# Kernel optimization log

Measured on AMD Instinct MI355X. Metric: run time of the kernel, lower is better.

The kernel has to match this reference:

```python
import jax, jax.numpy as jnp
import numpy as np

N, E = 50000, 800000
IN_DIM, HID, OUT_DIM = 512, 64, 40


def setup_inputs() -> dict:
    key = jax.random.key(0)
    ks = jax.random.split(key, 7)
    X = jax.random.normal(ks[0], (N, IN_DIM), dtype=jnp.float32)
    edges = jax.random.randint(ks[1], (2, E), 0, N, dtype=jnp.int64)
    # GCNConv weight (glorot) and bias
    W1 = jax.random.normal(ks[2], (IN_DIM, HID), dtype=jnp.float32) / np.sqrt(IN_DIM)
    b1 = jnp.zeros((HID,), dtype=jnp.float32)
    # fc Linear
    Wfc = jax.random.normal(ks[3], (OUT_DIM, HID), dtype=jnp.float32) / np.sqrt(HID)
    bfc = jax.random.normal(ks[4], (OUT_DIM,), dtype=jnp.float32) * 0.01
    return {"X": X, "edges": edges, "W1": W1, "b1": b1, "Wfc": Wfc, "bfc": bfc}


def gcn_conv(x, src, dst, W, b, n):
    # PyG GCNConv: transform, add self-loops, symmetric D^-1/2 A D^-1/2 norm,
    # scatter-add messages at destination, add bias.
    h = x @ W  # [N, HID]
    loop = jnp.arange(n, dtype=src.dtype)
    src = jnp.concatenate([src, loop])
    dst = jnp.concatenate([dst, loop])
    deg = jax.ops.segment_sum(jnp.ones_like(dst, dtype=h.dtype), dst, num_segments=n)
    dinv = jnp.where(deg > 0, jax.lax.rsqrt(deg), 0.0)
    coef = dinv[src] * dinv[dst]  # [E+N]
    msgs = coef[:, None] * h[src]  # gather + scale
    agg = jax.ops.segment_sum(msgs, dst, num_segments=n)  # scatter-add
    return agg + b


def reference(X, edges, W1, b1, Wfc, bfc):
    n = X.shape[0]
    src, dst = edges[0], edges[1]
    h = jax.nn.relu(gcn_conv(X, src, dst, W1, b1, n))  # [N, HID]
    return h @ Wfc.T + bfc  # [N, OUT_DIM]
```

## Files before the change

### kernel.cpp

```cpp
#include <hip/hip_runtime.h>
#include <hip/hip_bf16.h>

typedef unsigned short u16;
typedef __bf16 bf16_8 __attribute__((ext_vector_type(8)));
typedef float f32_4 __attribute__((ext_vector_type(4)));

#define IN_DIM 512
#define HID 64
#define OUT_DIM 40
#define CAP 64
#define CF_BLOCKS 512

__global__ void k_prep(const float* __restrict__ W1, u16* __restrict__ W1t,
                       int* __restrict__ cnt, int n) {
    int i = blockIdx.x * 256 + threadIdx.x;
    if (i < n) cnt[i] = 0;
    if (i < IN_DIM * HID) {
        int k = i / HID, o = i % HID;
        __hip_bfloat16 v = __float2bfloat16(W1[i]);
        W1t[o * IN_DIM + k] = *reinterpret_cast<u16*>(&v);
    }
}

__launch_bounds__(256)
__global__ void k_work(const float* __restrict__ X, const u16* __restrict__ W1t,
                       const int* __restrict__ src, const int* __restrict__ dst,
                       int* cnt, u16* __restrict__ csr, u16* __restrict__ hs,
                       int N, int E, int NT) {
    __shared__ __align__(16) u16 As[2][64 * 72];
    const int t = threadIdx.x;

    if ((int)blockIdx.x >= NT) {
        int tid = ((int)blockIdx.x - NT) * 256 + t;
        int stride = CF_BLOCKS * 256;
        for (int e = tid; e < E; e += stride) {
            int d = dst[e];
            int p = atomicAdd(&cnt[d], 1);
            if (p < CAP) csr[(size_t)d * CAP + p] = (u16)src[e];
        }
        return;
    }

    const int wave = t >> 6;
    const int lane = t & 63;
    const int m = lane & 15;
    const int quad = lane >> 4;
    const int n0 = blockIdx.x * 64;

    f32_4 acc[4];
    #pragma unroll
    for (int c = 0; c < 4; c++) acc[c] = (f32_4){0.f, 0.f, 0.f, 0.f};

    const int r_st = t >> 2;
    const int c2 = t & 3;

    int row = n0 + r_st; if (row >= N) row = N - 1;
    const float* xp = X + (size_t)row * IN_DIM + c2 * 16;

    f32_4 x0 = *reinterpret_cast<const f32_4*>(xp);
    f32_4 x1 = *reinterpret_cast<const f32_4*>(xp + 4);
    f32_4 x2 = *reinterpret_cast<const f32_4*>(xp + 8);
    f32_4 x3 = *reinterpret_cast<const f32_4*>(xp + 12);

    int buf = 0;
    for (int k0 = 0; k0 < IN_DIM; k0 += 64) {
        u16 xb[16];
        #pragma unroll
        for (int q = 0; q < 4; q++) {
            __hip_bfloat16 c0 = __float2bfloat16(x0[q]);
            __hip_bfloat16 c1 = __float2bfloat16(x1[q]);
            __hip_bfloat16 c2_ = __float2bfloat16(x2[q]);
            __hip_bfloat16 c3 = __float2bfloat16(x3[q]);
            xb[q]      = *reinterpret_cast<u16*>(&c0);
            xb[4 + q]  = *reinterpret_cast<u16*>(&c1);
            xb[8 + q]  = *reinterpret_cast<u16*>(&c2_);
            xb[12 + q] = *reinterpret_cast<u16*>(&c3);
        }
        u16* wp = &As[buf][r_st * 72 + c2 * 16];
        *reinterpret_cast<uint4*>(wp)     = *reinterpret_cast<uint4*>(&xb[0]);
        *reinterpret_cast<uint4*>(wp + 8) = *reinterpret_cast<uint4*>(&xb[8]);
        __syncthreads();

        if (k0 + 64 < IN_DIM) {
            x0 = *reinterpret_cast<const f32_4*>(xp + k0 + 64);
            x1 = *reinterpret_cast<const f32_4*>(xp + k0 + 68);
            x2 = *reinterpret_cast<const f32_4*>(xp + k0 + 72);
            x3 = *reinterpret_cast<const f32_4*>(xp + k0 + 76);
        }

        bf16_8 a0 = *reinterpret_cast<const bf16_8*>(&As[buf][(wave * 16 + m) * 72 + quad * 8]);
        bf16_8 a1 = *reinterpret_cast<const bf16_8*>(&As[buf][(wave * 16 + m) * 72 + 32 + quad * 8]);
        #pragma unroll
        for (int c = 0; c < 4; c++) {
            bf16_8 b0 = *reinterpret_cast<const bf16_8*>(
                W1t + (size_t)(c * 16 + m) * IN_DIM + k0 + quad * 8);
            bf16_8 b1 = *reinterpret_cast<const bf16_8*>(
                W1t + (size_t)(c * 16 + m) * IN_DIM + k0 + 32 + quad * 8);
            acc[c] = __builtin_amdgcn_mfma_f32_16x16x32_bf16(a0, b0, acc[c], 0, 0, 0);
            acc[c] = __builtin_amdgcn_mfma_f32_16x16x32_bf16(a1, b1, acc[c], 0, 0, 0);
        }
        __syncthreads();
        buf ^= 1;
    }

    const int nbase = n0 + wave * 16 + quad * 4;
    #pragma unroll
    for (int r = 0; r < 4; r++) {
        int n = nbase + r;
        if (n < N) {
            #pragma unroll
            for (int c = 0; c < 4; c++) {
                __hip_bfloat16 hv = __float2bfloat16(acc[c][r]);
                hs[(size_t)n * HID + c * 16 + m] = *reinterpret_cast<u16*>(&hv);
            }
        }
    }
}

__global__ void k_scale(u16* __restrict__ hs, const int* __restrict__ cnt, int N) {
    int i = blockIdx.x * 256 + threadIdx.x;
    int node = i >> 3;
    if (node >= N) return;
    float dv = rsqrtf((float)cnt[node] + 1.0f);
    uint4 v = *reinterpret_cast<uint4*>(hs + (size_t)i * 8);
    uint vv[4] = {v.x, v.y, v.z, v.w};
    u16 o[8];
    #pragma unroll
    for (int q = 0; q < 4; q++) {
        float lo = __uint_as_float(vv[q] << 16) * dv;
        float hi = __uint_as_float(vv[q] & 0xFFFF0000u) * dv;
        __hip_bfloat16 bl_ = __float2bfloat16(lo);
        __hip_bfloat16 bh_ = __float2bfloat16(hi);
        o[2 * q]     = *reinterpret_cast<u16*>(&bl_);
        o[2 * q + 1] = *reinterpret_cast<u16*>(&bh_);
    }
    *reinterpret_cast<uint4*>(hs + (size_t)i * 8) = *reinterpret_cast<uint4*>(o);
}

__device__ __forceinline__ void acc_add(f32_4& a, uint2 v) {
    a[0] += __uint_as_float(v.x << 16);
    a[1] += __uint_as_float(v.x & 0xFFFF0000u);
    a[2] += __uint_as_float(v.y << 16);
    a[3] += __uint_as_float(v.y & 0xFFFF0000u);
}

#define SHP 72

__launch_bounds__(256)
__global__ void k_aggfc(const u16* __restrict__ hs, const u16* __restrict__ csr,
                        const int* __restrict__ cnt, const float* __restrict__ b1,
                        const float* __restrict__ Wfc, const float* __restrict__ bfc,
                        float* __restrict__ out, int N) {
    __shared__ __align__(16) u16 shb[16 * SHP];
    __shared__ __align__(16) u16 wfb[48 * SHP];
    __shared__ float bl[48];
    const int t = threadIdx.x;

    for (int i = t; i < 48 * HID; i += 256) {
        int o = i / HID, k = i % HID;
        float v = (o < OUT_DIM) ? Wfc[o * HID + k] : 0.f;
        __hip_bfloat16 b = __float2bfloat16(v);
        wfb[o * SHP + k] = *reinterpret_cast<u16*>(&b);
    }
    if (t < 48) bl[t] = (t < OUT_DIM) ? bfc[t] : 0.f;

    const int g = t >> 4, l = t & 15;
    const int n = blockIdx.x * 16 + g;

    if (n < N) {
        const uint2* hs2 = reinterpret_cast<const uint2*>(hs);
        f32_4 aa[4];
        #pragma unroll
        for (int q = 0; q < 4; q++) aa[q] = (f32_4){0.f, 0.f, 0.f, 0.f};
        const float dvn = rsqrtf((float)cnt[n] + 1.0f);
        acc_add(aa[0], hs2[(size_t)n * 16 + l]);
        int deg = cnt[n]; if (deg > CAP) deg = CAP;
        uint2 cv = reinterpret_cast<const uint2*>(csr + (size_t)n * CAP)[l];
        const int nn1 = N - 1;
        for (int j = 0; j < deg; j += 16) {
            int base = j >> 2;
            uint wx[4], wy[4];
            #pragma unroll
            for (int q = 0; q < 4; q++) {
                wx[q] = __shfl(cv.x, base + q, 16);
                wy[q] = __shfl(cv.y, base + q, 16);
            }
            int s[16];
            #pragma unroll
            for (int q = 0; q < 4; q++) {
                s[4 * q + 0] = (int)(wx[q] & 0xffff);
                s[4 * q + 1] = (int)(wx[q] >> 16);
                s[4 * q + 2] = (int)(wy[q] & 0xffff);
                s[4 * q + 3] = (int)(wy[q] >> 16);
            }
            uint2 v[16];
            #pragma unroll
            for (int i = 0; i < 16; i++) {
                int si = s[i] < nn1 ? s[i] : nn1;
                v[i] = hs2[(size_t)si * 16 + l];
            }
            #pragma unroll
            for (int i = 0; i < 16; i++) {
                if (j + i >= deg) { v[i].x = 0u; v[i].y = 0u; }
                acc_add(aa[i & 3], v[i]);
            }
        }
        f32_4 acc = (aa[0] + aa[1]) + (aa[2] + aa[3]);
        u16 rb[4];
        #pragma unroll
        for (int q = 0; q < 4; q++) {
            float x = dvn * acc[q] + b1[l * 4 + q];
            x = x > 0.f ? x : 0.f;
            __hip_bfloat16 hb = __float2bfloat16(x);
            rb[q] = *reinterpret_cast<u16*>(&hb);
        }
        *reinterpret_cast<uint2*>(&shb[g * SHP + l * 4]) = *reinterpret_cast<uint2*>(rb);
    }
    __syncthreads();

    const int wave = t >> 6;
    const int lane = t & 63;
    const int m = lane & 15;
    const int quad = lane >> 4;
    if (wave < 3) {
        bf16_8 a0 = *reinterpret_cast<const bf16_8*>(&shb[m * SHP + quad * 8]);
        bf16_8 a1 = *reinterpret_cast<const bf16_8*>(&shb[m * SHP + 32 + quad * 8]);
        bf16_8 b0 = *reinterpret_cast<const bf16_8*>(&wfb[(wave * 16 + m) * SHP + quad * 8]);
        bf16_8 b1 = *reinterpret_cast<const bf16_8*>(&wfb[(wave * 16 + m) * SHP + 32 + quad * 8]);
        f32_4 c = (f32_4){0.f, 0.f, 0.f, 0.f};
        c = __builtin_amdgcn_mfma_f32_16x16x32_bf16(a0, b0, c, 0, 0, 0);
        c = __builtin_amdgcn_mfma_f32_16x16x32_bf16(a1, b1, c, 0, 0, 0);
        const int o = wave * 16 + m;
        if (o < OUT_DIM) {
            const int base = blockIdx.x * 16;
            #pragma unroll
            for (int r = 0; r < 4; r++) {
                int node = base + quad * 4 + r;
                if (node < N) out[(size_t)node * OUT_DIM + o] = c[r] + bl[o];
            }
        }
    }
}


extern "C" void kernel_launch(void* const* d_in, const int* in_sizes, int n_in,
                              void* d_out, int out_size, void* d_ws, size_t ws_size,
                              hipStream_t stream) {
    const float* X   = (const float*)d_in[0];
    const int* edges = (const int*)d_in[1];
    const float* W1  = (const float*)d_in[2];
    const float* b1  = (const float*)d_in[3];
    const float* Wfc = (const float*)d_in[4];
    const float* bfc = (const float*)d_in[5];

    const int N = in_sizes[0] / IN_DIM;
    const int E = in_sizes[1] / 2;
    const int* src = edges;
    const int* dst = edges + E;

    char* p = (char*)d_ws;
    auto carve = [&](size_t bytes) -> char* {
        char* r = p;
        p += (bytes + 255) & ~(size_t)255;
        return r;
    };
    u16* W1t = (u16*)carve((size_t)IN_DIM * HID * 2);
    u16* hs  = (u16*)carve((size_t)N * HID * 2);
    int* cnt = (int*)carve((size_t)N * 4);
    u16* csr = (u16*)carve((size_t)N * CAP * 2);

    const int nb = (N + 255) / 256;
    const int NT = (N + 63) / 64;

    k_prep <<<nb, 256, 0, stream>>>(W1, W1t, cnt, N);
    k_work <<<NT + CF_BLOCKS, 256, 0, stream>>>(X, W1t, src, dst, cnt, csr, hs, N, E, NT);
    k_scale<<<(N * 8 + 255) / 256, 256, 0, stream>>>(hs, cnt, N);
    k_aggfc<<<(N + 15) / 16, 256, 0, stream>>>(hs, csr, cnt, b1, Wfc, bfc,
                                               (float*)d_out, N);
}
```

Before: 233.3 us.

## Load X fragments directly into MFMA registers, drop LDS staging; unroll CSR fill

The GEMM path no longer stages X tiles through shared memory with block barriers. Each lane loads its own MFMA A-fragment straight from global memory, converts it to bf16 in registers and prefetches the next k-chunk. The CSR-building blocks double in count and process two edges per iteration so more atomics are in flight. The trade-off is less coalesced 32-byte-per-lane global reads of X and extra redundant loads, in exchange for removing LDS traffic and syncthreads.

```diff
diff --git a/kernel.cpp b/kernel.cpp
--- a/kernel.cpp
+++ b/kernel.cpp
@@ -9,7 +9,7 @@
 #define HID 64
 #define OUT_DIM 40
 #define CAP 64
-#define CF_BLOCKS 512
+#define CF_BLOCKS 1024
 
 __global__ void k_prep(const float* __restrict__ W1, u16* __restrict__ W1t,
                        int* __restrict__ cnt, int n) {
@@ -27,13 +27,21 @@
                        const int* __restrict__ src, const int* __restrict__ dst,
                        int* cnt, u16* __restrict__ csr, u16* __restrict__ hs,
                        int N, int E, int NT) {
-    __shared__ __align__(16) u16 As[2][64 * 72];
     const int t = threadIdx.x;
 
     if ((int)blockIdx.x >= NT) {
         int tid = ((int)blockIdx.x - NT) * 256 + t;
-        int stride = CF_BLOCKS * 256;
-        for (int e = tid; e < E; e += stride) {
+        const int stride = CF_BLOCKS * 256;
+        int e = tid;
+        for (; e + stride < E; e += 2 * stride) {
+            int d0 = dst[e], d1 = dst[e + stride];
+            int s0 = src[e], s1 = src[e + stride];
+            int p0 = atomicAdd(&cnt[d0], 1);
+            int p1 = atomicAdd(&cnt[d1], 1);
+            if (p0 < CAP) csr[(size_t)d0 * CAP + p0] = (u16)s0;
+            if (p1 < CAP) csr[(size_t)d1 * CAP + p1] = (u16)s1;
+        }
+        for (; e < E; e += stride) {
             int d = dst[e];
             int p = atomicAdd(&cnt[d], 1);
             if (p < CAP) csr[(size_t)d * CAP + p] = (u16)src[e];
@@ -47,60 +55,57 @@
     const int quad = lane >> 4;
     const int n0 = blockIdx.x * 64;
 
+    int row = n0 + wave * 16 + m; if (row >= N) row = N - 1;
+    const float* xp = X + (size_t)row * IN_DIM + quad * 8;
+    const u16* bp = W1t + (size_t)m * IN_DIM + quad * 8;
+
     f32_4 acc[4];
     #pragma unroll
     for (int c = 0; c < 4; c++) acc[c] = (f32_4){0.f, 0.f, 0.f, 0.f};
 
-    const int r_st = t >> 2;
-    const int c2 = t & 3;
-
-    int row = n0 + r_st; if (row >= N) row = N - 1;
-    const float* xp = X + (size_t)row * IN_DIM + c2 * 16;
-
-    f32_4 x0 = *reinterpret_cast<const f32_4*>(xp);
-    f32_4 x1 = *reinterpret_cast<const f32_4*>(xp + 4);
-    f32_4 x2 = *reinterpret_cast<const f32_4*>(xp + 8);
-    f32_4 x3 = *reinterpret_cast<const f32_4*>(xp + 12);
-
-    int buf = 0;
+    f32_4 xa0 = *reinterpret_cast<const f32_4*>(xp);
+    f32_4 xa1 = *reinterpret_cast<const f32_4*>(xp + 4);
+    f32_4 xb0 = *reinterpret_cast<const f32_4*>(xp + 32);
+    f32_4 xb1 = *reinterpret_cast<const f32_4*>(xp + 36);
+
     for (int k0 = 0; k0 < IN_DIM; k0 += 64) {
-        u16 xb[16];
+        union { bf16_8 v; u16 s[8]; } au;
         #pragma unroll
         for (int q = 0; q < 4; q++) {
-            __hip_bfloat16 c0 = __float2bfloat16(x0[q]);
-            __hip_bfloat16 c1 = __float2bfloat16(x1[q]);
-            __hip_bfloat16 c2_ = __float2bfloat16(x2[q]);
-            __hip_bfloat16 c3 = __float2bfloat16(x3[q]);
-            xb[q]      = *reinterpret_cast<u16*>(&c0);
-            xb[4 + q]  = *reinterpret_cast<u16*>(&c1);
-            xb[8 + q]  = *reinterpret_cast<u16*>(&c2_);
-            xb[12 + q] = *reinterpret_cast<u16*>(&c3);
-        }
-        u16* wp = &As[buf][r_st * 72 + c2 * 16];
-        *reinterpret_cast<uint4*>(wp)     = *reinterpret_cast<uint4*>(&xb[0]);
-        *reinterpret_cast<uint4*>(wp + 8) = *reinterpret_cast<uint4*>(&xb[8]);
-        __syncthreads();
-
-        if (k0 + 64 < IN_DIM) {
-            x0 = *reinterpret_cast<const f32_4*>(xp + k0 + 64);
-            x1 = *reinterpret_cast<const f32_4*>(xp + k0 + 68);
-            x2 = *reinterpret_cast<const f32_4*>(xp + k0 + 72);
-            x3 = *reinterpret_cast<const f32_4*>(xp + k0 + 76);
-        }
-
-        bf16_8 a0 = *reinterpret_cast<const bf16_8*>(&As[buf][(wave * 16 + m) * 72 + quad * 8]);
-        bf16_8 a1 = *reinterpret_cast<const bf16_8*>(&As[buf][(wave * 16 + m) * 72 + 32 + quad * 8]);
+            __hip_bfloat16 c0 = __float2bfloat16(xa0[q]);
+            __hip_bfloat16 c1 = __float2bfloat16(xa1[q]);
+            au.s[q]     = *reinterpret_cast<u16*>(&c0);
+            au.s[4 + q] = *reinterpret_cast<u16*>(&c1);
+        }
+        {
+            int kn = k0 + 64; if (kn >= IN_DIM) kn = 0;
+            xa0 = *reinterpret_cast<const f32_4*>(xp + kn);
+            xa1 = *reinterpret_cast<const f32_4*>(xp + kn + 4);
+        }
         #pragma unroll
         for (int c = 0; c < 4; c++) {
-            bf16_8 b0 = *reinterpret_cast<const bf16_8*>(
-                W1t + (size_t)(c * 16 + m) * IN_DIM + k0 + quad * 8);
-            bf16_8 b1 = *reinterpret_cast<const bf16_8*>(
-                W1t + (size_t)(c * 16 + m) * IN_DIM + k0 + 32 + quad * 8);
-            acc[c] = __builtin_amdgcn_mfma_f32_16x16x32_bf16(a0, b0, acc[c], 0, 0, 0);
-            acc[c] = __builtin_amdgcn_mfma_f32_16x16x32_bf16(a1, b1, acc[c], 0, 0, 0);
-        }
-        __syncthreads();
-        buf ^= 1;
+            bf16_8 b = *reinterpret_cast<const bf16_8*>(bp + (size_t)c * 16 * IN_DIM + k0);
+            acc[c] = __builtin_amdgcn_mfma_f32_16x16x32_bf16(au.v, b, acc[c], 0, 0, 0);
+        }
+
+        union { bf16_8 v; u16 s[8]; } av;
+        #pragma unroll
+        for (int q = 0; q < 4; q++) {
+            __hip_bfloat16 c0 = __float2bfloat16(xb0[q]);
+            __hip_bfloat16 c1 = __float2bfloat16(xb1[q]);
+            av.s[q]     = *reinterpret_cast<u16*>(&c0);
+            av.s[4 + q] = *reinterpret_cast<u16*>(&c1);
+        }
+        {
+            int kn = k0 + 96; if (kn >= IN_DIM) kn = 32;
+            xb0 = *reinterpret_cast<const f32_4*>(xp + kn);
+            xb1 = *reinterpret_cast<const f32_4*>(xp + kn + 4);
+        }
+        #pragma unroll
+        for (int c = 0; c < 4; c++) {
+            bf16_8 b = *reinterpret_cast<const bf16_8*>(bp + (size_t)c * 16 * IN_DIM + k0 + 32);
+            acc[c] = __builtin_amdgcn_mfma_f32_16x16x32_bf16(av.v, b, acc[c], 0, 0, 0);
+        }
     }
 
     const int nbase = n0 + wave * 16 + quad * 4;
```

Measured after the change: 241.3 us. +3.4%, slower.
